# Performance work log

Hardware: AMD Instinct MI355X
Metric: run time of the kernel (lower is better)

The kernel has to match this reference:

```python
import jax, jax.numpy as jnp
import numpy as np

B, S, H = 2, 1024, 2048
NH, NKV, D = 16, 4, 128
E, K, F = 16, 2, 1408          # routed experts, top_k, moe_intermediate
FS = 1408                      # shared-expert intermediate (n_shared_experts=1)
EPS = 1e-5
RSF = 1.0                      # routed_scaling_factor


def rmsnorm(x, w):
    v = jnp.mean(jnp.square(x.astype(jnp.float32)), axis=-1, keepdims=True)
    return (x * jax.lax.rsqrt(v + EPS)).astype(x.dtype) * w


def rotate_half(x):
    x1, x2 = jnp.split(x, 2, axis=-1)
    return jnp.concatenate([-x2, x1], axis=-1)


def apply_rope(x, cos, sin):
    # x: [B,S,h,D]; cos/sin: [S,D]
    c = cos[None, :, None, :]
    s = sin[None, :, None, :]
    return x * c + rotate_half(x) * s


def setup_inputs() -> dict:
    key = jax.random.key(0)
    ks = jax.random.split(key, 16)
    sc = 0.02
    hidden_states = jax.random.normal(ks[0], (B, S, H), dtype=jnp.float32)
    # rotary embedding tables
    inv_freq = 1.0 / (10000.0 ** (np.arange(0, D, 2, dtype=np.float32) / D))
    ang = np.arange(S, dtype=np.float32)[:, None] * inv_freq[None, :]
    emb = np.concatenate([ang, ang], axis=-1)
    cos = jnp.asarray(np.cos(emb), dtype=jnp.float32)
    sin = jnp.asarray(np.sin(emb), dtype=jnp.float32)
    return {
        'hidden_states': hidden_states,
        'cos': cos,
        'sin': sin,
        'ln1_w': jnp.ones((H,), jnp.float32),
        'ln2_w': jnp.ones((H,), jnp.float32),
        'q_norm_w': jnp.ones((D,), jnp.float32),
        'k_norm_w': jnp.ones((D,), jnp.float32),
        'wq': jax.random.normal(ks[1], (H, NH * D), jnp.float32) * sc,
        'wk': jax.random.normal(ks[2], (H, NKV * D), jnp.float32) * sc,
        'wv': jax.random.normal(ks[3], (H, NKV * D), jnp.float32) * sc,
        'wo': jax.random.normal(ks[4], (NH * D, H), jnp.float32) * sc,
        'gate_w': jax.random.normal(ks[5], (E, H), jnp.float32) * sc,
        'expert_gate_up': jax.random.normal(ks[6], (E, H, 2 * F), jnp.float32) * sc,
        'expert_down': jax.random.normal(ks[7], (E, F, H), jnp.float32) * sc,
        'shared_gate_up': jax.random.normal(ks[8], (H, 2 * FS), jnp.float32) * sc,
        'shared_down': jax.random.normal(ks[9], (FS, H), jnp.float32) * sc,
    }


def silu_and_mul(gu):
    g, u = jnp.split(gu, 2, axis=-1)
    return jax.nn.silu(g) * u


def moe_block(tokens, gate_w, expert_gate_up, expert_down, shared_gate_up, shared_down):
    # tokens: [T,H]
    T = tokens.shape[0]
    router_logits = tokens.astype(jnp.float32) @ gate_w.T          # [T,E]
    probs = jax.nn.softmax(router_logits, axis=-1)
    topk_w, topk_ids = jax.lax.top_k(probs, K)                     # [T,K]
    topk_w = topk_w / jnp.sum(topk_w, axis=-1, keepdims=True)      # renormalize
    # dense combine-weight matrix [T,E] (top_k sparse routing)
    cw = jnp.zeros((T, E), jnp.float32).at[jnp.arange(T)[:, None], topk_ids].add(topk_w)
    # scan over experts: each expert is a full SwiGLU MLP on all tokens, masked by cw
    def body(acc, we):
        gw, dw, cwe = we                                            # [H,2F],[F,H],[T]
        y = silu_and_mul(tokens @ gw) @ dw                          # [T,H]
        return acc + cwe[:, None].astype(y.dtype) * y, None
    out, _ = jax.lax.scan(body, jnp.zeros_like(tokens), (expert_gate_up, expert_down, cw.T))
    out = out * RSF
    shared = silu_and_mul(tokens @ shared_gate_up) @ shared_down
    return out + shared


def reference(hidden_states, cos, sin, ln1_w, ln2_w, q_norm_w, k_norm_w,
              wq, wk, wv, wo, gate_w, expert_gate_up, expert_down,
              shared_gate_up, shared_down):
    # input layernorm (residual=None branch)
    residual = hidden_states
    x = rmsnorm(hidden_states, ln1_w)
    # attention
    q = (x @ wq).reshape(B, S, NH, D)
    k = (x @ wk).reshape(B, S, NKV, D)
    v = (x @ wv).reshape(B, S, NKV, D)
    q = rmsnorm(q, q_norm_w)
    k = rmsnorm(k, k_norm_w)
    q = apply_rope(q, cos, sin)
    k = apply_rope(k, cos, sin)
    rep = NH // NKV
    k = jnp.repeat(k, rep, axis=2)
    v = jnp.repeat(v, rep, axis=2)
    scores = jnp.einsum('bihd,bjhd->bhij', q, k) / jnp.sqrt(jnp.float32(D))
    causal = jnp.tril(jnp.ones((S, S), bool))
    scores = jnp.where(causal[None, None], scores, -jnp.inf)
    attn = jax.nn.softmax(scores, axis=-1)
    o = jnp.einsum('bhij,bjhd->bihd', attn, v).reshape(B, S, NH * D)
    attn_out = o @ wo
    # post-attention layernorm with fused residual add
    residual = residual + attn_out
    x = rmsnorm(residual, ln2_w)
    # MoE + shared expert
    tokens = x.reshape(-1, H)
    out = moe_block(tokens, gate_w, expert_gate_up, expert_down, shared_gate_up, shared_down)
    hidden = out.reshape(B, S, H)
    return hidden, residual
```

## Files before the change

kernel.cpp:

```cpp
#include <hip/hip_runtime.h>
#include <stdint.h>

typedef unsigned short u16;
typedef unsigned int   u32;
typedef __attribute__((ext_vector_type(4))) float     f32x4;
typedef __attribute__((ext_vector_type(8))) _Float16  f16x8;

#define S_LEN 1024
#define NB    2
#define H_DIM 2048
#define T_TOK 2048
#define NHEAD 16
#define NKVH  4
#define DHEAD 128
#define NEXP  16
#define FFE   1408
#define FF2   2816
#define EPSF  1e-5f
#define RSF_C 1.0f

__device__ __forceinline__ u16 f2h(float f){
  _Float16 h = (_Float16)f;
  return __builtin_bit_cast(unsigned short, h);
}
__device__ __forceinline__ void split2(float f, u16& hi, u16& lo){
  _Float16 h = (_Float16)f;
  hi = __builtin_bit_cast(unsigned short, h);
  _Float16 l = (_Float16)((f - (float)h) * 2048.0f);
  lo = __builtin_bit_cast(unsigned short, l);
}
__device__ __forceinline__ void gload_lds16(const void* g, void* l){
  __builtin_amdgcn_global_load_lds((const __attribute__((address_space(1))) void*)g,
                                   (__attribute__((address_space(3))) void*)l, 16, 0, 0);
}
__device__ __forceinline__ uint4 pack8(const u16* p){
  return make_uint4((u32)p[0] | ((u32)p[1]<<16), (u32)p[2] | ((u32)p[3]<<16),
                    (u32)p[4] | ((u32)p[5]<<16), (u32)p[6] | ((u32)p[7]<<16));
}

__global__ __launch_bounds__(256) void tsplit_all_kernel(
    const float* __restrict__ wq, const float* __restrict__ wk,
    const float* __restrict__ wv, const float* __restrict__ wo,
    const float* __restrict__ sgu, const float* __restrict__ sdn,
    u16* __restrict__ wqkvh, u16* __restrict__ wqkvl,
    u16* __restrict__ woh,  u16* __restrict__ wol,
    u16* __restrict__ sgut, u16* __restrict__ sdnt)
{
  const int z = blockIdx.z;
  const float* in; int ldn; u16* outh; u16* outl; int ldk, nx, ny; bool dual;
  switch (z) {
    case 0:  in=wq;  ldn=2048; outh=wqkvh;              outl=wqkvl;              ldk=2048; nx=32; ny=32; dual=true;  break;
    case 1:  in=wk;  ldn=512;  outh=wqkvh+2048*2048;    outl=wqkvl+2048*2048;    ldk=2048; nx=8;  ny=32; dual=true;  break;
    case 2:  in=wv;  ldn=512;  outh=wqkvh+2560*2048;    outl=wqkvl+2560*2048;    ldk=2048; nx=8;  ny=32; dual=true;  break;
    case 3:  in=wo;  ldn=2048; outh=woh;                outl=wol;                ldk=2048; nx=32; ny=32; dual=true;  break;
    case 4:  in=sgu; ldn=2816; outh=sgut;               outl=nullptr;            ldk=2048; nx=44; ny=32; dual=false; break;
    default: in=sdn; ldn=2048; outh=sdnt;               outl=nullptr;            ldk=1408; nx=32; ny=22; dual=false; break;
  }
  if ((int)blockIdx.x >= nx || (int)blockIdx.y >= ny) return;
  __shared__ float tile[64][65];
  const int n0 = blockIdx.x * 64, k0 = blockIdx.y * 64;
  const int tid = threadIdx.x;
  const int tr = tid >> 4, tc = (tid & 15) * 4;
  #pragma unroll
  for (int i = 0; i < 4; i++) {
    float4 v = *(const float4*)&in[(size_t)(k0 + tr + i*16) * ldn + (n0 + tc)];
    tile[tr + i*16][tc+0] = v.x; tile[tr + i*16][tc+1] = v.y;
    tile[tr + i*16][tc+2] = v.z; tile[tr + i*16][tc+3] = v.w;
  }
  __syncthreads();
  const int n = tid >> 2, kg = (tid & 3) * 16;
  u16 hb[16], lb[16];
  #pragma unroll
  for (int j = 0; j < 16; j++) {
    float f = tile[kg + j][n];
    if (dual) split2(f, hb[j], lb[j]); else hb[j] = f2h(f);
  }
  u16* dh = &outh[(size_t)(n0 + n) * ldk + k0 + kg];
  *(uint4*)dh       = pack8(hb);
  *(uint4*)(dh + 8) = pack8(hb + 8);
  if (dual) {
    u16* dl = &outl[(size_t)(n0 + n) * ldk + k0 + kg];
    *(uint4*)dl       = pack8(lb);
    *(uint4*)(dl + 8) = pack8(lb + 8);
  }
}

__global__ __launch_bounds__(256) void rmsnorm_kernel(
    const float* __restrict__ in, const float* __restrict__ w,
    u16* __restrict__ outh, u16* __restrict__ outl)
{
  __shared__ float red[4];
  const int t = blockIdx.x, tid = threadIdx.x;
  const int lane = tid & 63, wave = tid >> 6;
  const float* x = in + (size_t)t * H_DIM;
  const int c = tid * 8;
  float4 v0 = *(const float4*)&x[c];
  float4 v1 = *(const float4*)&x[c + 4];
  float ss = v0.x*v0.x + v0.y*v0.y + v0.z*v0.z + v0.w*v0.w
           + v1.x*v1.x + v1.y*v1.y + v1.z*v1.z + v1.w*v1.w;
  #pragma unroll
  for (int d = 1; d < 64; d <<= 1) ss += __shfl_xor(ss, d, 64);
  if (lane == 0) red[wave] = ss;
  __syncthreads();
  float rinv = rsqrtf((red[0]+red[1]+red[2]+red[3]) * (1.0f/H_DIM) + EPSF);
  float4 w0 = *(const float4*)&w[c];
  float4 w1 = *(const float4*)&w[c + 4];
  float vals[8] = { v0.x*rinv*w0.x, v0.y*rinv*w0.y, v0.z*rinv*w0.z, v0.w*rinv*w0.w,
                    v1.x*rinv*w1.x, v1.y*rinv*w1.y, v1.z*rinv*w1.z, v1.w*rinv*w1.w };
  u16 hb[8], lb[8];
  #pragma unroll
  for (int j = 0; j < 8; j++) split2(vals[j], hb[j], lb[j]);
  *(uint4*)&outh[(size_t)t * H_DIM + c] = pack8(hb);
  if (outl) *(uint4*)&outl[(size_t)t * H_DIM + c] = pack8(lb);
}

__global__ __launch_bounds__(256) void gemm3b_kernel(
    const u16* __restrict__ Ah, const u16* __restrict__ Al, int lda,
    const u16* __restrict__ Bh, const u16* __restrict__ Bl, int ldb,
    float* __restrict__ C, int ldc,
    const float* __restrict__ addsrc, int K)
{
  __shared__ u16 Ash[128*64], Asl[128*64];
  __shared__ u16 Bsh[128*64], Bsl[128*64];
  const int tid = threadIdx.x, lane = tid & 63, wave = tid >> 6;
  const int m0 = blockIdx.y * 128, n0 = blockIdx.x * 128;
  const int wm = (wave >> 1) * 64, wn = (wave & 1) * 64;
  const int arow = lane >> 3;
  const int acol = ((lane & 7) ^ arow) * 8;
  f32x4 acc0[4][4] = {}, acc1[4][4] = {};
  for (int k0 = 0; k0 < K; k0 += 64) {
    #pragma unroll
    for (int g = 0; g < 4; g++) {
      const int rb = wave*32 + g*8;
      gload_lds16(Ah + (size_t)(m0 + rb + arow)*lda + k0 + acol, &Ash[rb*64]);
      gload_lds16(Al + (size_t)(m0 + rb + arow)*lda + k0 + acol, &Asl[rb*64]);
      gload_lds16(Bh + (size_t)(n0 + rb + arow)*ldb + k0 + acol, &Bsh[rb*64]);
      gload_lds16(Bl + (size_t)(n0 + rb + arow)*ldb + k0 + acol, &Bsl[rb*64]);
    }
    asm volatile("s_waitcnt vmcnt(0) lgkmcnt(0)" ::: "memory");
    __syncthreads();
    const int fr = lane & 15, fg = lane >> 4;
    #pragma unroll
    for (int kk = 0; kk < 2; kk++) {
      const int cb = fg + kk*4;
      f16x8 ah[4], al[4];
      #pragma unroll
      for (int m = 0; m < 4; m++) {
        const int r = wm + m*16 + fr;
        const int s = (cb ^ (r & 7)) * 8;
        ah[m] = *(const f16x8*)&Ash[r*64 + s];
        al[m] = *(const f16x8*)&Asl[r*64 + s];
      }
      #pragma unroll
      for (int n = 0; n < 4; n++) {
        const int r = wn + n*16 + fr;
        const int s = (cb ^ (r & 7)) * 8;
        f16x8 bh_ = *(const f16x8*)&Bsh[r*64 + s];
        f16x8 bl_ = *(const f16x8*)&Bsl[r*64 + s];
        #pragma unroll
        for (int m = 0; m < 4; m++) {
          acc0[m][n] = __builtin_amdgcn_mfma_f32_16x16x32_f16(ah[m], bh_, acc0[m][n], 0,0,0);
          acc1[m][n] = __builtin_amdgcn_mfma_f32_16x16x32_f16(ah[m], bl_, acc1[m][n], 0,0,0);
          acc1[m][n] = __builtin_amdgcn_mfma_f32_16x16x32_f16(al[m], bh_, acc1[m][n], 0,0,0);
        }
      }
    }
    __syncthreads();
  }
  const int cr = (lane >> 4) * 4, cc = lane & 15;
  #pragma unroll
  for (int m = 0; m < 4; m++)
    #pragma unroll
    for (int n = 0; n < 4; n++)
      #pragma unroll
      for (int j = 0; j < 4; j++) {
        int r = m0 + wm + m*16 + cr + j;
        size_t idx = (size_t)r * ldc + (n0 + wn + n*16 + cc);
        float v = acc0[m][n][j] + acc1[m][n][j] * (1.0f/2048.0f);
        if (addsrc) v += addsrc[idx];
        C[idx] = v;
      }
}

__global__ __launch_bounds__(256) void gemm_up_all_kernel(
    const int* __restrict__ list, const float* __restrict__ egu, float* __restrict__ gu_exp,
    const int* __restrict__ counts, const int* __restrict__ offs,
    const int* __restrict__ tile_e, const int* __restrict__ tile_m0,
    const u16* __restrict__ tok, const u16* __restrict__ sgut, float* __restrict__ gu_sh)
{
  __shared__ u16 As[256*64];
  __shared__ u16 Bs[64*64];
  const int z = blockIdx.z;
  const int tid = threadIdx.x, lane = tid & 63, wave = tid >> 6;
  const int n0 = blockIdx.x * 64;
  const int wm = wave * 64;
  const int arow = lane >> 3;
  const int acol = ((lane & 7) ^ arow) * 8;
  const int fr = lane & 15, fg = lane >> 4;
  const int cr = (lane >> 4) * 4, cc = lane & 15;

  if (z < 32) {
    const int e = tile_e[z];
    if (e < 0) return;
    const int m0 = tile_m0[z];
    const int cnt = counts[e];
    const int off = offs[e];
    const float* B = egu + (size_t)e * H_DIM * FF2;
    float* C = gu_exp + (size_t)off * FF2;
    const u16* arp[8];
    #pragma unroll
    for (int g = 0; g < 8; g++) {
      int idx = off + m0 + wm + g*8 + arow;
      if (idx > 2*T_TOK - 1) idx = 2*T_TOK - 1;
      arp[g] = tok + (size_t)list[idx] * H_DIM + acol;
    }
    const int bn  = tid & 63;
    const int bkb = tid >> 6;
    const int bs0 = bn*64 + (((bkb*2)     ^ (bn & 7)) * 8);
    const int bs1 = bn*64 + (((bkb*2 + 1) ^ (bn & 7)) * 8);
    f32x4 acc[4][4] = {};
    for (int k0 = 0; k0 < H_DIM; k0 += 64) {
      #pragma unroll
      for (int g = 0; g < 8; g++)
        gload_lds16(arp[g] + k0, &As[(wm + g*8)*64]);
      {
        const float* gb = B + (size_t)(k0 + bkb*16) * FF2 + (n0 + bn);
        float f[16];
        #pragma unroll
        for (int j = 0; j < 16; j++) f[j] = gb[(size_t)j * FF2];
        u32 pk[8];
        #pragma unroll
        for (int j = 0; j < 8; j++)
          pk[j] = __builtin_bit_cast(u32, __builtin_amdgcn_cvt_pkrtz(f[2*j], f[2*j+1]));
        *(uint4*)&Bs[bs0] = make_uint4(pk[0], pk[1], pk[2], pk[3]);
        *(uint4*)&Bs[bs1] = make_uint4(pk[4], pk[5], pk[6], pk[7]);
      }
      asm volatile("s_waitcnt vmcnt(0) lgkmcnt(0)" ::: "memory");
      __syncthreads();
      #pragma unroll
      for (int kk = 0; kk < 2; kk++) {
        const int cb = fg + kk*4;
        f16x8 a[4], b[4];
        #pragma unroll
        for (int m = 0; m < 4; m++) {
          const int r = wm + m*16 + fr;
          a[m] = *(const f16x8*)&As[r*64 + ((cb ^ (r & 7)) * 8)];
        }
        #pragma unroll
        for (int n = 0; n < 4; n++) {
          const int r = n*16 + fr;
          b[n] = *(const f16x8*)&Bs[r*64 + ((cb ^ (r & 7)) * 8)];
        }
        #pragma unroll
        for (int n = 0; n < 4; n++)
          #pragma unroll
          for (int m = 0; m < 4; m++)
            acc[m][n] = __builtin_amdgcn_mfma_f32_16x16x32_f16(a[m], b[n], acc[m][n], 0,0,0);
      }
      __syncthreads();
    }
    #pragma unroll
    for (int m = 0; m < 4; m++)
      #pragma unroll
      for (int n = 0; n < 4; n++)
        #pragma unroll
        for (int j = 0; j < 4; j++) {
          int r = m0 + wm + m*16 + cr + j;
          if (r < cnt) C[(size_t)r * FF2 + (n0 + n*16 + cc)] = acc[m][n][j];
        }
  } else {
    const int m0 = (z - 32) * 256;
    f32x4 acc[4][4] = {};
    for (int k0 = 0; k0 < H_DIM; k0 += 64) {
      #pragma unroll
      for (int g = 0; g < 8; g++)
        gload_lds16(tok + (size_t)(m0 + wm + g*8 + arow)*H_DIM + k0 + acol,
                    &As[(wm + g*8)*64]);
      #pragma unroll
      for (int g = 0; g < 2; g++)
        gload_lds16(sgut + (size_t)(n0 + wave*16 + g*8 + arow)*H_DIM + k0 + acol,
                    &Bs[(wave*16 + g*8)*64]);
      asm volatile("s_waitcnt vmcnt(0) lgkmcnt(0)" ::: "memory");
      __syncthreads();
      #pragma unroll
      for (int kk = 0; kk < 2; kk++) {
        const int cb = fg + kk*4;
        f16x8 a[4], b[4];
        #pragma unroll
        for (int m = 0; m < 4; m++) {
          const int r = wm + m*16 + fr;
          a[m] = *(const f16x8*)&As[r*64 + ((cb ^ (r & 7)) * 8)];
        }
        #pragma unroll
        for (int n = 0; n < 4; n++) {
          const int r = n*16 + fr;
          b[n] = *(const f16x8*)&Bs[r*64 + ((cb ^ (r & 7)) * 8)];
        }
        #pragma unroll
        for (int n = 0; n < 4; n++)
          #pragma unroll
          for (int m = 0; m < 4; m++)
            acc[m][n] = __builtin_amdgcn_mfma_f32_16x16x32_f16(a[m], b[n], acc[m][n], 0,0,0);
      }
      __syncthreads();
    }
    #pragma unroll
    for (int m = 0; m < 4; m++)
      #pragma unroll
      for (int n = 0; n < 4; n++)
        #pragma unroll
        for (int j = 0; j < 4; j++)
          gu_sh[(size_t)(m0 + wm + m*16 + cr + j) * FF2 + (n0 + n*16 + cc)] = acc[m][n][j];
  }
}

__global__ __launch_bounds__(256) void gemm_dn_all_kernel(
    const u16* __restrict__ Aexp, const float* __restrict__ edn, float* __restrict__ y_exp,
    const int* __restrict__ counts, const int* __restrict__ offs,
    const int* __restrict__ tile_e, const int* __restrict__ tile_m0,
    const u16* __restrict__ act_sh, const u16* __restrict__ sdnt, float* __restrict__ out_sh)
{
  __shared__ u16 As[256*64];
  __shared__ u16 Bs[64*64];
  const int z = blockIdx.z;
  const int tid = threadIdx.x, lane = tid & 63, wave = tid >> 6;
  const int n0 = blockIdx.x * 64;
  const int wm = wave * 64;
  const int arow = lane >> 3;
  const int acol = ((lane & 7) ^ arow) * 8;
  const int fr = lane & 15, fg = lane >> 4;
  const int cr = (lane >> 4) * 4, cc = lane & 15;

  if (z < 32) {
    const int e = tile_e[z];
    if (e < 0) return;
    const int m0 = tile_m0[z];
    const int cnt = counts[e];
    const int off = offs[e];
    const u16* A = Aexp + (size_t)off * FFE;
    const float* B = edn + (size_t)e * FFE * H_DIM;
    float* C = y_exp + (size_t)off * H_DIM;
    const int bn  = tid & 63;
    const int bkb = tid >> 6;
    const int bs0 = bn*64 + (((bkb*2)     ^ (bn & 7)) * 8);
    const int bs1 = bn*64 + (((bkb*2 + 1) ^ (bn & 7)) * 8);
    f32x4 acc[4][4] = {};
    for (int k0 = 0; k0 < FFE; k0 += 64) {
      #pragma unroll
      for (int g = 0; g < 8; g++)
        gload_lds16(A + (size_t)(m0 + wm + g*8 + arow)*FFE + k0 + acol,
                    &As[(wm + g*8)*64]);
      {
        const float* gb = B + (size_t)(k0 + bkb*16) * H_DIM + (n0 + bn);
        float f[16];
        #pragma unroll
        for (int j = 0; j < 16; j++) f[j] = gb[(size_t)j * H_DIM];
        u32 pk[8];
        #pragma unroll
        for (int j = 0; j < 8; j++)
          pk[j] = __builtin_bit_cast(u32, __builtin_amdgcn_cvt_pkrtz(f[2*j], f[2*j+1]));
        *(uint4*)&Bs[bs0] = make_uint4(pk[0], pk[1], pk[2], pk[3]);
        *(uint4*)&Bs[bs1] = make_uint4(pk[4], pk[5], pk[6], pk[7]);
      }
      asm volatile("s_waitcnt vmcnt(0) lgkmcnt(0)" ::: "memory");
      __syncthreads();
      #pragma unroll
      for (int kk = 0; kk < 2; kk++) {
        const int cb = fg + kk*4;
        f16x8 a[4], b[4];
        #pragma unroll
        for (int m = 0; m < 4; m++) {
          const int r = wm + m*16 + fr;
          a[m] = *(const f16x8*)&As[r*64 + ((cb ^ (r & 7)) * 8)];
        }
        #pragma unroll
        for (int n = 0; n < 4; n++) {
          const int r = n*16 + fr;
          b[n] = *(const f16x8*)&Bs[r*64 + ((cb ^ (r & 7)) * 8)];
        }
        #pragma unroll
        for (int n = 0; n < 4; n++)
          #pragma unroll
          for (int m = 0; m < 4; m++)
            acc[m][n] = __builtin_amdgcn_mfma_f32_16x16x32_f16(a[m], b[n], acc[m][n], 0,0,0);
      }
      __syncthreads();
    }
    #pragma unroll
    for (int m = 0; m < 4; m++)
      #pragma unroll
      for (int n = 0; n < 4; n++)
        #pragma unroll
        for (int j = 0; j < 4; j++) {
          int r = m0 + wm + m*16 + cr + j;
          if (r < cnt) C[(size_t)r * H_DIM + (n0 + n*16 + cc)] = acc[m][n][j];
        }
  } else {
    const int m0 = (z - 32) * 256;
    f32x4 acc[4][4] = {};
    for (int k0 = 0; k0 < FFE; k0 += 64) {
      #pragma unroll
      for (int g = 0; g < 8; g++)
        gload_lds16(act_sh + (size_t)(m0 + wm + g*8 + arow)*FFE + k0 + acol,
                    &As[(wm + g*8)*64]);
      #pragma unroll
      for (int g = 0; g < 2; g++)
        gload_lds16(sdnt + (size_t)(n0 + wave*16 + g*8 + arow)*FFE + k0 + acol,
                    &Bs[(wave*16 + g*8)*64]);
      asm volatile("s_waitcnt vmcnt(0) lgkmcnt(0)" ::: "memory");
      __syncthreads();
      #pragma unroll
      for (int kk = 0; kk < 2; kk++) {
        const int cb = fg + kk*4;
        f16x8 a[4], b[4];
        #pragma unroll
        for (int m = 0; m < 4; m++) {
          const int r = wm + m*16 + fr;
          a[m] = *(const f16x8*)&As[r*64 + ((cb ^ (r & 7)) * 8)];
        }
        #pragma unroll
        for (int n = 0; n < 4; n++) {
          const int r = n*16 + fr;
          b[n] = *(const f16x8*)&Bs[r*64 + ((cb ^ (r & 7)) * 8)];
        }
        #pragma unroll
        for (int n = 0; n < 4; n++)
          #pragma unroll
          for (int m = 0; m < 4; m++)
            acc[m][n] = __builtin_amdgcn_mfma_f32_16x16x32_f16(a[m], b[n], acc[m][n], 0,0,0);
      }
      __syncthreads();
    }
    #pragma unroll
    for (int m = 0; m < 4; m++)
      #pragma unroll
      for (int n = 0; n < 4; n++)
        #pragma unroll
        for (int j = 0; j < 4; j++)
          out_sh[(size_t)(m0 + wm + m*16 + cr + j) * H_DIM + (n0 + n*16 + cc)] = acc[m][n][j];
  }
}

__global__ __launch_bounds__(256) void rope_kernel(
    const float* __restrict__ qkv,
    const float* __restrict__ cosb, const float* __restrict__ sinb,
    const float* __restrict__ qnw, const float* __restrict__ knw,
    u16* __restrict__ qrh, u16* __restrict__ qrl,
    u16* __restrict__ krh, u16* __restrict__ krl,
    u16* __restrict__ vth, u16* __restrict__ vtl)
{
  const int jid = blockIdx.x * 4 + (threadIdx.x >> 6);
  const int lane = threadIdx.x & 63;
  const int t = jid / 24, r = jid - t*24;
  const int b = t >> 10, s = t & (S_LEN - 1);
  const float* row = qkv + (size_t)t * 3072;
  if (r < NHEAD + NKVH) {
    const bool isq = (r < NHEAD);
    const int h = isq ? r : (r - NHEAD);
    const float* x = row + (isq ? h*DHEAD : (2048 + h*DHEAD));
    const float* nw = isq ? qnw : knw;
    float x0 = x[lane], x1 = x[lane + 64];
    float ss = x0*x0 + x1*x1;
    #pragma unroll
    for (int d = 1; d < 64; d <<= 1) ss += __shfl_xor(ss, d, 64);
    float rinv = rsqrtf(ss * (1.0f/DHEAD) + EPSF);
    float n0 = x0*rinv*nw[lane], n1 = x1*rinv*nw[lane + 64];
    float o0 = n0*cosb[s*DHEAD + lane]      - n1*sinb[s*DHEAD + lane];
    float o1 = n1*cosb[s*DHEAD + lane + 64] + n0*sinb[s*DHEAD + lane + 64];
    size_t base = isq ? ((size_t)(b*NHEAD + h)*S_LEN + s)*DHEAD
                      : ((size_t)(b*NKVH + h)*S_LEN + s)*DHEAD;
    u16* dh = isq ? qrh : krh;
    u16* dl = isq ? qrl : krl;
    u16 hh, ll;
    split2(o0, hh, ll); dh[base + lane]      = hh; dl[base + lane]      = ll;
    split2(o1, hh, ll); dh[base + lane + 64] = hh; dl[base + lane + 64] = ll;
  } else {
    const int h = r - NHEAD - NKVH;
    const float* x = row + 2560 + h*DHEAD;
    size_t base = (size_t)(b*NKVH + h)*DHEAD*S_LEN + s;
    u16 hh, ll;
    split2(x[lane], hh, ll);
    vth[base + (size_t)lane*S_LEN] = hh; vtl[base + (size_t)lane*S_LEN] = ll;
    split2(x[lane + 64], hh, ll);
    vth[base + (size_t)(lane + 64)*S_LEN] = hh; vtl[base + (size_t)(lane + 64)*S_LEN] = ll;
  }
}

__global__ __launch_bounds__(256) void attn_kernel(
    const u16* __restrict__ qrh, const u16* __restrict__ qrl,
    const u16* __restrict__ krh, const u16* __restrict__ krl,
    const u16* __restrict__ vth, const u16* __restrict__ vtl,
    u16* __restrict__ oh, u16* __restrict__ ol)
{
  __shared__ u16 Kh[64*128], Kl[64*128];
  __shared__ u16 Vh[128*64], Vl[128*64];
  __shared__ u16 Ph[4*16*64], Pl[4*16*64];
  const int bx = blockIdx.x, h = blockIdx.y, b = blockIdx.z;
  const int hkv = h >> 2;
  const int lane = threadIdx.x & 63, wave = threadIdx.x >> 6;
  const int fr = lane & 15, fg = lane >> 4;
  const u16* qbh = qrh + ((size_t)(b*NHEAD + h)*S_LEN)*DHEAD;
  const u16* qbl = qrl + ((size_t)(b*NHEAD + h)*S_LEN)*DHEAD;
  const u16* kbh = krh + ((size_t)(b*NKVH + hkv)*S_LEN)*DHEAD;
  const u16* kbl = krl + ((size_t)(b*NKVH + hkv)*S_LEN)*DHEAD;
  const u16* vbh = vth + ((size_t)(b*NKVH + hkv)*DHEAD)*S_LEN;
  const u16* vbl = vtl + ((size_t)(b*NKVH + hkv)*DHEAD)*S_LEN;
  const float scl = 0.08838834764831845f;

  for (int it = 0; it < 2; it++) {
    const int qt = it ? (15 - bx) : bx;
    const int q0 = qt * 64;
    f16x8 aqh[4], aql[4];
    {
      const size_t qrow = (size_t)(q0 + wave*16 + fr)*DHEAD;
      #pragma unroll
      for (int kk = 0; kk < 4; kk++) {
        aqh[kk] = *(const f16x8*)&qbh[qrow + kk*32 + fg*8];
        aql[kk] = *(const f16x8*)&qbl[qrow + kk*32 + fg*8];
      }
    }
    f32x4 o0[8] = {}, o1[8] = {};
    float mrow[4] = {-1e30f,-1e30f,-1e30f,-1e30f};
    float lrow[4] = {0.f,0.f,0.f,0.f};
    for (int jt = 0; jt <= qt; jt++) {
      const int j0 = jt * 64;
      #pragma unroll
      for (int p = 0; p < 4; p++) {
        const int ck = p*4 + wave;
        gload_lds16(kbh + (size_t)(j0 + ck*4 + (lane>>4))*DHEAD + (lane&15)*8, &Kh[ck*512]);
        gload_lds16(kbl + (size_t)(j0 + ck*4 + (lane>>4))*DHEAD + (lane&15)*8, &Kl[ck*512]);
        gload_lds16(vbh + (size_t)(ck*8 + (lane>>3))*S_LEN + j0 + (lane&7)*8, &Vh[ck*512]);
        gload_lds16(vbl + (size_t)(ck*8 + (lane>>3))*S_LEN + j0 + (lane&7)*8, &Vl[ck*512]);
      }
      __syncthreads();
      f32x4 s0[4] = {}, s1[4] = {};
      #pragma unroll
      for (int kk = 0; kk < 4; kk++) {
        const int ko = kk*32 + fg*8;
        #pragma unroll
        for (int n = 0; n < 4; n++) {
          f16x8 bh_ = *(const f16x8*)&Kh[(n*16 + fr)*128 + ko];
          f16x8 bl_ = *(const f16x8*)&Kl[(n*16 + fr)*128 + ko];
          s0[n] = __builtin_amdgcn_mfma_f32_16x16x32_f16(aqh[kk], bh_, s0[n], 0,0,0);
          s1[n] = __builtin_amdgcn_mfma_f32_16x16x32_f16(aqh[kk], bl_, s1[n], 0,0,0);
          s1[n] = __builtin_amdgcn_mfma_f32_16x16x32_f16(aql[kk], bh_, s1[n], 0,0,0);
        }
      }
      const int rb = q0 + wave*16 + fg*4;
      float pv[4][4];
      #pragma unroll
      for (int n = 0; n < 4; n++)
        #pragma unroll
        for (int j = 0; j < 4; j++) {
          float v = (s0[n][j] + s1[n][j]*(1.0f/2048.0f)) * scl;
          if (j0 + n*16 + fr > rb + j) v = -1e30f;
          pv[n][j] = v;
        }
      float alpha[4];
      #pragma unroll
      for (int j = 0; j < 4; j++) {
        float mx = fmaxf(fmaxf(pv[0][j], pv[1][j]), fmaxf(pv[2][j], pv[3][j]));
        #pragma unroll
        for (int d = 1; d < 16; d <<= 1) mx = fmaxf(mx, __shfl_xor(mx, d, 64));
        float mnew = fmaxf(mrow[j], mx);
        alpha[j] = __expf(mrow[j] - mnew);
        mrow[j] = mnew;
      }
      float rsum[4] = {0.f,0.f,0.f,0.f};
      #pragma unroll
      for (int n = 0; n < 4; n++)
        #pragma unroll
        for (int j = 0; j < 4; j++) {
          float p = __expf(pv[n][j] - mrow[j]);
          pv[n][j] = p;
          rsum[j] += p;
        }
      #pragma unroll
      for (int j = 0; j < 4; j++) {
        #pragma unroll
        for (int d = 1; d < 16; d <<= 1) rsum[j] += __shfl_xor(rsum[j], d, 64);
        lrow[j] = lrow[j]*alpha[j] + rsum[j];
      }
      #pragma unroll
      for (int n2 = 0; n2 < 8; n2++)
        #pragma unroll
        for (int j = 0; j < 4; j++) { o0[n2][j] *= alpha[j]; o1[n2][j] *= alpha[j]; }
      #pragma unroll
      for (int n = 0; n < 4; n++)
        #pragma unroll
        for (int j = 0; j < 4; j++) {
          u16 hh, ll; split2(pv[n][j], hh, ll);
          Ph[wave*1024 + (fg*4 + j)*64 + n*16 + fr] = hh;
          Pl[wave*1024 + (fg*4 + j)*64 + n*16 + fr] = ll;
        }
      __syncthreads();
      #pragma unroll
      for (int kk = 0; kk < 2; kk++) {
        const int ko = kk*32 + fg*8;
        f16x8 ah_ = *(const f16x8*)&Ph[wave*1024 + fr*64 + ko];
        f16x8 al_ = *(const f16x8*)&Pl[wave*1024 + fr*64 + ko];
        #pragma unroll
        for (int n2 = 0; n2 < 8; n2++) {
          f16x8 vh_ = *(const f16x8*)&Vh[(n2*16 + fr)*64 + ko];
          f16x8 vl_ = *(const f16x8*)&Vl[(n2*16 + fr)*64 + ko];
          o0[n2] = __builtin_amdgcn_mfma_f32_16x16x32_f16(ah_, vh_, o0[n2], 0,0,0);
          o1[n2] = __builtin_amdgcn_mfma_f32_16x16x32_f16(ah_, vl_, o1[n2], 0,0,0);
          o1[n2] = __builtin_amdgcn_mfma_f32_16x16x32_f16(al_, vh_, o1[n2], 0,0,0);
        }
      }
      __syncthreads();
    }
    float inv[4];
    #pragma unroll
    for (int j = 0; j < 4; j++) inv[j] = 1.0f / lrow[j];
    #pragma unroll
    for (int n2 = 0; n2 < 8; n2++)
      #pragma unroll
      for (int j = 0; j < 4; j++) {
        int s = q0 + wave*16 + fg*4 + j;
        size_t idx = ((size_t)(b*S_LEN + s))*H_DIM + h*DHEAD + n2*16 + fr;
        float val = (o0[n2][j] + o1[n2][j]*(1.0f/2048.0f)) * inv[j];
        u16 hh, ll; split2(val, hh, ll);
        oh[idx] = hh; ol[idx] = ll;
      }
  }
}

__global__ __launch_bounds__(64) void router_kernel(
    const float* __restrict__ resid, const float* __restrict__ ln2w,
    const float* __restrict__ gw, int* __restrict__ ids, float* __restrict__ wts,
    int* __restrict__ counts)
{
  const int t = blockIdx.x, lane = threadIdx.x;
  const float* x = resid + (size_t)t * H_DIM;
  float xv[32];
  float ss = 0.f;
  #pragma unroll
  for (int p = 0; p < 8; p++) {
    float4 v  = *(const float4*)&x[p*256 + lane*4];
    float4 lw = *(const float4*)&ln2w[p*256 + lane*4];
    ss += v.x*v.x + v.y*v.y + v.z*v.z + v.w*v.w;
    xv[p*4+0] = v.x*lw.x; xv[p*4+1] = v.y*lw.y; xv[p*4+2] = v.z*lw.z; xv[p*4+3] = v.w*lw.w;
  }
  #pragma unroll
  for (int d = 1; d < 64; d <<= 1) ss += __shfl_xor(ss, d, 64);
  const float rinv = rsqrtf(ss * (1.0f/H_DIM) + EPSF);
  float lg[NEXP];
  #pragma unroll
  for (int e = 0; e < NEXP; e++) {
    const float* g = gw + (size_t)e * H_DIM;
    float dacc = 0.f;
    #pragma unroll
    for (int p = 0; p < 8; p++) {
      float4 gv = *(const float4*)&g[p*256 + lane*4];
      dacc += xv[p*4+0]*gv.x + xv[p*4+1]*gv.y + xv[p*4+2]*gv.z + xv[p*4+3]*gv.w;
    }
    #pragma unroll
    for (int d = 1; d < 64; d <<= 1) dacc += __shfl_xor(dacc, d, 64);
    lg[e] = dacc * rinv;
  }
  if (lane == 0) {
    int i0 = 0; float b0 = lg[0];
    #pragma unroll
    for (int e = 1; e < NEXP; e++) if (lg[e] > b0) { b0 = lg[e]; i0 = e; }
    int i1 = -1; float b1 = -3e38f;
    #pragma unroll
    for (int e = 0; e < NEXP; e++) if (e != i0 && lg[e] > b1) { b1 = lg[e]; i1 = e; }
    float rr = __expf(b1 - b0);
    float w0 = 1.0f / (1.0f + rr);
    ids[t*2] = i0; ids[t*2+1] = i1;
    wts[t*2] = w0; wts[t*2+1] = rr * w0;
    atomicAdd(&counts[i0], 1);
    atomicAdd(&counts[i1], 1);
  }
}

__global__ void scan_kernel(const int* __restrict__ counts, int* __restrict__ offs,
                            int* __restrict__ cursor,
                            int* __restrict__ tile_e, int* __restrict__ tile_m0)
{
  if (threadIdx.x == 0) {
    int s = 0, nt = 0;
    for (int e = 0; e < NEXP; e++) {
      offs[e] = s; cursor[e] = 0;
      int c = counts[e];
      for (int m0 = 0; m0 < c; m0 += 256) { tile_e[nt] = e; tile_m0[nt] = m0; nt++; }
      s += c;
    }
    for (; nt < 32; nt++) { tile_e[nt] = -1; tile_m0[nt] = 0; }
  }
}

__global__ __launch_bounds__(256) void scatter_kernel(
    const int* __restrict__ ids, const int* __restrict__ offs,
    int* __restrict__ cursor, int* __restrict__ list, int* __restrict__ pos)
{
  int t = blockIdx.x * 256 + threadIdx.x;
  if (t < T_TOK) {
    for (int kk = 0; kk < 2; kk++) {
      int e = ids[t*2 + kk];
      int p = atomicAdd(&cursor[e], 1);
      int i = offs[e] + p;
      list[i] = t;
      pos[t*2 + kk] = i;
    }
  }
}

__global__ __launch_bounds__(256) void silu_all_kernel(
    const float* __restrict__ gu_exp, u16* __restrict__ act_ex,
    const float* __restrict__ gu_sh,  u16* __restrict__ act_sh)
{
  const int rr = blockIdx.x;
  const float* g;
  u16* o;
  if (rr < 2*T_TOK) { g = gu_exp + (size_t)rr * FF2;          o = act_ex + (size_t)rr * FFE; }
  else              { g = gu_sh  + (size_t)(rr - 2*T_TOK) * FF2; o = act_sh + (size_t)(rr - 2*T_TOK) * FFE; }
  for (int c = threadIdx.x*4; c < FFE; c += 1024) {
    float4 gv = *(const float4*)&g[c];
    float4 uv = *(const float4*)&g[c + FFE];
    float s0 = gv.x / (1.0f + __expf(-gv.x)) * uv.x;
    float s1 = gv.y / (1.0f + __expf(-gv.y)) * uv.y;
    float s2 = gv.z / (1.0f + __expf(-gv.z)) * uv.z;
    float s3 = gv.w / (1.0f + __expf(-gv.w)) * uv.w;
    u32 lo = (u32)f2h(s0) | ((u32)f2h(s1) << 16);
    u32 hi = (u32)f2h(s2) | ((u32)f2h(s3) << 16);
    *(uint2*)&o[c] = make_uint2(lo, hi);
  }
}

__global__ __launch_bounds__(256) void combine_kernel(
    const float* __restrict__ y,
    const int* __restrict__ pos, const float* __restrict__ wts,
    float* __restrict__ out)
{
  const int t = blockIdx.x;
  const int p0 = pos[t*2], p1 = pos[t*2+1];
  const float w0 = wts[t*2] * RSF_C, w1 = wts[t*2+1] * RSF_C;
  const int c = threadIdx.x * 8;
  #pragma unroll
  for (int q = 0; q < 2; q++) {
    const int cc = c + q*4;
    float4 s  = *(const float4*)&out[(size_t)t*H_DIM + cc];
    float4 a  = *(const float4*)&y[(size_t)p0*H_DIM + cc];
    float4 bb = *(const float4*)&y[(size_t)p1*H_DIM + cc];
    float4 r;
    r.x = s.x + w0*a.x + w1*bb.x;
    r.y = s.y + w0*a.y + w1*bb.y;
    r.z = s.z + w0*a.z + w1*bb.z;
    r.w = s.w + w0*a.w + w1*bb.w;
    *(float4*)&out[(size_t)t*H_DIM + cc] = r;
  }
}

extern "C" void kernel_launch(void* const* d_in, const int* in_sizes, int n_in,
                              void* d_out, int out_size, void* d_ws, size_t ws_size,
                              hipStream_t stream)
{
  (void)in_sizes; (void)n_in; (void)out_size;
  const float* hidden = (const float*)d_in[0];
  const float* cosb   = (const float*)d_in[1];
  const float* sinb   = (const float*)d_in[2];
  const float* ln1w   = (const float*)d_in[3];
  const float* ln2w   = (const float*)d_in[4];
  const float* qnw    = (const float*)d_in[5];
  const float* knw    = (const float*)d_in[6];
  const float* wq     = (const float*)d_in[7];
  const float* wk     = (const float*)d_in[8];
  const float* wv     = (const float*)d_in[9];
  const float* wo     = (const float*)d_in[10];
  const float* gw     = (const float*)d_in[11];
  const float* egu    = (const float*)d_in[12];
  const float* edn    = (const float*)d_in[13];
  const float* sgu    = (const float*)d_in[14];
  const float* sdn    = (const float*)d_in[15];
  float* out_hidden = (float*)d_out;
  float* resid = (float*)d_out + (size_t)T_TOK * H_DIM;

  char* ws = (char*)d_ws;
  constexpr size_t OFF_XH    = 0;
  constexpr size_t OFF_XL    = 8388608;
  constexpr size_t OFF_WQKVH = 16777216;
  constexpr size_t OFF_WQKVL = 29360128;
  constexpr size_t OFF_WOH   = 41943040;
  constexpr size_t OFF_WOL   = 50331648;
  constexpr size_t OFF_QKV   = 58720256;
  constexpr size_t OFF_QRH = 16777216, OFF_QRL = 25165824;
  constexpr size_t OFF_KRH = 33554432, OFF_KRL = 35651584;
  constexpr size_t OFF_VTH = 37748736, OFF_VTL = 39845888;
  constexpr size_t OFF_OH = 58720256, OFF_OL = 67108864;
  constexpr size_t OFF_GUE = 0;
  constexpr size_t OFF_TOK = 63963136;
  constexpr size_t OFF_ACE = 72351744;
  constexpr size_t OFF_GUS = 84606976;
  constexpr size_t OFF_ACS = 107675648;
  constexpr size_t OFF_SGUT= 113442816;
  constexpr size_t OFF_SDNT= 124977152;
  constexpr size_t OFF_IDS = 130744320;
  constexpr size_t OFF_WTS = OFF_IDS + 16384;
  constexpr size_t OFF_POS = OFF_WTS + 16384;
  constexpr size_t OFF_LST = OFF_POS + 16384;
  constexpr size_t OFF_CNT = OFF_LST + 16384;
  constexpr size_t OFF_OFS = OFF_CNT + 64;
  constexpr size_t OFF_CUR = OFF_OFS + 64;
  constexpr size_t OFF_TE  = OFF_CUR + 64;
  constexpr size_t OFF_TM  = OFF_TE + 128;
  constexpr size_t WS_NEED = OFF_TM + 128;
  if (ws_size < WS_NEED) return;

  u16* xh     = (u16*)(ws + OFF_XH);
  u16* xl     = (u16*)(ws + OFF_XL);
  u16* wqkvh  = (u16*)(ws + OFF_WQKVH);
  u16* wqkvl  = (u16*)(ws + OFF_WQKVL);
  u16* woh    = (u16*)(ws + OFF_WOH);
  u16* wol    = (u16*)(ws + OFF_WOL);
  float* qkv  = (float*)(ws + OFF_QKV);
  u16* q_rh = (u16*)(ws + OFF_QRH);
  u16* q_rl = (u16*)(ws + OFF_QRL);
  u16* k_rh = (u16*)(ws + OFF_KRH);
  u16* k_rl = (u16*)(ws + OFF_KRL);
  u16* v_th = (u16*)(ws + OFF_VTH);
  u16* v_tl = (u16*)(ws + OFF_VTL);
  u16* o_h  = (u16*)(ws + OFF_OH);
  u16* o_l  = (u16*)(ws + OFF_OL);
  float* gu_exp = (float*)(ws + OFF_GUE);
  float* y_exp  = (float*)(ws + OFF_GUE);
  u16* tok      = (u16*)(ws + OFF_TOK);
  u16* act_ex   = (u16*)(ws + OFF_ACE);
  float* gu_sh  = (float*)(ws + OFF_GUS);
  u16* act_sh   = (u16*)(ws + OFF_ACS);
  u16* sgut     = (u16*)(ws + OFF_SGUT);
  u16* sdnt     = (u16*)(ws + OFF_SDNT);
  int* ids    = (int*)(ws + OFF_IDS);
  float* wts  = (float*)(ws + OFF_WTS);
  int* pos    = (int*)(ws + OFF_POS);
  int* list   = (int*)(ws + OFF_LST);
  int* counts = (int*)(ws + OFF_CNT);
  int* offs   = (int*)(ws + OFF_OFS);
  int* cursor = (int*)(ws + OFF_CUR);
  int* tile_e = (int*)(ws + OFF_TE);
  int* tile_m0= (int*)(ws + OFF_TM);

  hipMemsetAsync(counts, 0, 64, stream);

  tsplit_all_kernel<<<dim3(44,32,6), 256, 0, stream>>>(wq, wk, wv, wo, sgu, sdn,
                                                       wqkvh, wqkvl, woh, wol, sgut, sdnt);

  rmsnorm_kernel<<<T_TOK, 256, 0, stream>>>(hidden, ln1w, xh, xl);
  gemm3b_kernel<<<dim3(24,16), 256, 0, stream>>>(xh, xl, H_DIM, wqkvh, wqkvl, 2048, qkv, 3072, nullptr, H_DIM);
  rope_kernel<<<(T_TOK*24)/4, 256, 0, stream>>>(qkv, cosb, sinb, qnw, knw,
                                                q_rh, q_rl, k_rh, k_rl, v_th, v_tl);
  attn_kernel<<<dim3(8, NHEAD, NB), 256, 0, stream>>>(q_rh, q_rl, k_rh, k_rl, v_th, v_tl, o_h, o_l);
  gemm3b_kernel<<<dim3(16,16), 256, 0, stream>>>(o_h, o_l, H_DIM, woh, wol, 2048, resid, H_DIM, hidden, H_DIM);

  rmsnorm_kernel<<<T_TOK, 256, 0, stream>>>(resid, ln2w, tok, nullptr);
  router_kernel<<<T_TOK, 64, 0, stream>>>(resid, ln2w, gw, ids, wts, counts);
  scan_kernel<<<1, 64, 0, stream>>>(counts, offs, cursor, tile_e, tile_m0);
  scatter_kernel<<<8, 256, 0, stream>>>(ids, offs, cursor, list, pos);

  gemm_up_all_kernel<<<dim3(44,1,40), 256, 0, stream>>>(list, egu, gu_exp,
                                                        counts, offs, tile_e, tile_m0,
                                                        tok, sgut, gu_sh);
  silu_all_kernel<<<3*T_TOK, 256, 0, stream>>>(gu_exp, act_ex, gu_sh, act_sh);
  gemm_dn_all_kernel<<<dim3(32,1,40), 256, 0, stream>>>(act_ex, edn, y_exp,
                                                        counts, offs, tile_e, tile_m0,
                                                        act_sh, sdnt, out_hidden);
  combine_kernel<<<T_TOK, 256, 0, stream>>>(y_exp, pos, wts, out_hidden);
}
```

Before: 737.6 us.

## Overlap wo and shared-expert weight conversion with attention in one launch

The weight transpose/split work for wo and the shared-expert matrices moves out of the upfront conversion kernel and into extra z-slices of the attention launch, so it runs alongside the 256 attention blocks, which alone underfill the GPU. The upfront kernel now converts only wq/wk/wv. The goal is to fill idle CUs during attention and shorten the serial prologue. In exchange, the merged kernel uses the larger 80KB shared-memory footprint for every block, which can lower occupancy for the conversion blocks. The launch grid also contains many early-exit blocks.

```diff
diff --git a/kernel.cpp b/kernel.cpp
--- a/kernel.cpp
+++ b/kernel.cpp
@@ -38,26 +38,12 @@
                     (u32)p[4] | ((u32)p[5]<<16), (u32)p[6] | ((u32)p[7]<<16));
 }
 
-__global__ __launch_bounds__(256) void tsplit_all_kernel(
-    const float* __restrict__ wq, const float* __restrict__ wk,
-    const float* __restrict__ wv, const float* __restrict__ wo,
-    const float* __restrict__ sgu, const float* __restrict__ sdn,
-    u16* __restrict__ wqkvh, u16* __restrict__ wqkvl,
-    u16* __restrict__ woh,  u16* __restrict__ wol,
-    u16* __restrict__ sgut, u16* __restrict__ sdnt)
-{
-  const int z = blockIdx.z;
-  const float* in; int ldn; u16* outh; u16* outl; int ldk, nx, ny; bool dual;
-  switch (z) {
-    case 0:  in=wq;  ldn=2048; outh=wqkvh;              outl=wqkvl;              ldk=2048; nx=32; ny=32; dual=true;  break;
-    case 1:  in=wk;  ldn=512;  outh=wqkvh+2048*2048;    outl=wqkvl+2048*2048;    ldk=2048; nx=8;  ny=32; dual=true;  break;
-    case 2:  in=wv;  ldn=512;  outh=wqkvh+2560*2048;    outl=wqkvl+2560*2048;    ldk=2048; nx=8;  ny=32; dual=true;  break;
-    case 3:  in=wo;  ldn=2048; outh=woh;                outl=wol;                ldk=2048; nx=32; ny=32; dual=true;  break;
-    case 4:  in=sgu; ldn=2816; outh=sgut;               outl=nullptr;            ldk=2048; nx=44; ny=32; dual=false; break;
-    default: in=sdn; ldn=2048; outh=sdnt;               outl=nullptr;            ldk=1408; nx=32; ny=22; dual=false; break;
-  }
-  if ((int)blockIdx.x >= nx || (int)blockIdx.y >= ny) return;
-  __shared__ float tile[64][65];
+__device__ __forceinline__ void tsplit_body(
+    const float* __restrict__ in, int ldn,
+    u16* __restrict__ outh, u16* __restrict__ outl, int ldk, bool dual,
+    void* smem)
+{
+  float (*tile)[65] = (float(*)[65])smem;
   const int n0 = blockIdx.x * 64, k0 = blockIdx.y * 64;
   const int tid = threadIdx.x;
   const int tr = tid >> 4, tc = (tid & 15) * 4;
@@ -83,6 +69,23 @@
     *(uint4*)dl       = pack8(lb);
     *(uint4*)(dl + 8) = pack8(lb + 8);
   }
+}
+
+__global__ __launch_bounds__(256) void tsplit_all_kernel(
+    const float* __restrict__ wq, const float* __restrict__ wk,
+    const float* __restrict__ wv,
+    u16* __restrict__ wqkvh, u16* __restrict__ wqkvl)
+{
+  const int z = blockIdx.z;
+  const float* in; int ldn; u16* outh; u16* outl; int nx;
+  switch (z) {
+    case 0:  in=wq;  ldn=2048; outh=wqkvh;            outl=wqkvl;            nx=32; break;
+    case 1:  in=wk;  ldn=512;  outh=wqkvh+2048*2048;  outl=wqkvl+2048*2048;  nx=8;  break;
+    default: in=wv;  ldn=512;  outh=wqkvh+2560*2048;  outl=wqkvl+2560*2048;  nx=8;  break;
+  }
+  if ((int)blockIdx.x >= nx) return;
+  __shared__ __align__(16) char smem[16704];
+  tsplit_body(in, ldn, outh, outl, 2048, true, smem);
 }
 
 __global__ __launch_bounds__(256) void rmsnorm_kernel(
@@ -486,16 +489,36 @@
   }
 }
 
-__global__ __launch_bounds__(256) void attn_kernel(
+__global__ __launch_bounds__(256) void attn_mix_kernel(
     const u16* __restrict__ qrh, const u16* __restrict__ qrl,
     const u16* __restrict__ krh, const u16* __restrict__ krl,
     const u16* __restrict__ vth, const u16* __restrict__ vtl,
-    u16* __restrict__ oh, u16* __restrict__ ol)
-{
-  __shared__ u16 Kh[64*128], Kl[64*128];
-  __shared__ u16 Vh[128*64], Vl[128*64];
-  __shared__ u16 Ph[4*16*64], Pl[4*16*64];
-  const int bx = blockIdx.x, h = blockIdx.y, b = blockIdx.z;
+    u16* __restrict__ oh, u16* __restrict__ ol,
+    const float* __restrict__ wo, const float* __restrict__ sgu, const float* __restrict__ sdn,
+    u16* __restrict__ woh, u16* __restrict__ wol,
+    u16* __restrict__ sgut, u16* __restrict__ sdnt)
+{
+  __shared__ __align__(16) char smem[81920];
+  const int z = blockIdx.z;
+  if (z >= 2) {
+    const float* in; int ldn; u16* outh; u16* outl; int ldk, nx, ny; bool dual;
+    switch (z) {
+      case 2:  in=wo;  ldn=2048; outh=woh;  outl=wol;     ldk=2048; nx=32; ny=32; dual=true;  break;
+      case 3:  in=sgu; ldn=2816; outh=sgut; outl=nullptr; ldk=2048; nx=44; ny=32; dual=false; break;
+      default: in=sdn; ldn=2048; outh=sdnt; outl=nullptr; ldk=1408; nx=32; ny=22; dual=false; break;
+    }
+    if ((int)blockIdx.x >= nx || (int)blockIdx.y >= ny) return;
+    tsplit_body(in, ldn, outh, outl, ldk, dual, smem);
+    return;
+  }
+  if ((int)blockIdx.x >= 8 || (int)blockIdx.y >= NHEAD) return;
+  u16* Kh = (u16*)smem;
+  u16* Kl = (u16*)(smem + 16384);
+  u16* Vh = (u16*)(smem + 32768);
+  u16* Vl = (u16*)(smem + 49152);
+  u16* Ph = (u16*)(smem + 65536);
+  u16* Pl = (u16*)(smem + 73728);
+  const int bx = blockIdx.x, h = blockIdx.y, b = z;
   const int hkv = h >> 2;
   const int lane = threadIdx.x & 63, wave = threadIdx.x >> 6;
   const int fr = lane & 15, fg = lane >> 4;
@@ -843,14 +866,14 @@
 
   hipMemsetAsync(counts, 0, 64, stream);
 
-  tsplit_all_kernel<<<dim3(44,32,6), 256, 0, stream>>>(wq, wk, wv, wo, sgu, sdn,
-                                                       wqkvh, wqkvl, woh, wol, sgut, sdnt);
+  tsplit_all_kernel<<<dim3(32,32,3), 256, 0, stream>>>(wq, wk, wv, wqkvh, wqkvl);
 
   rmsnorm_kernel<<<T_TOK, 256, 0, stream>>>(hidden, ln1w, xh, xl);
   gemm3b_kernel<<<dim3(24,16), 256, 0, stream>>>(xh, xl, H_DIM, wqkvh, wqkvl, 2048, qkv, 3072, nullptr, H_DIM);
   rope_kernel<<<(T_TOK*24)/4, 256, 0, stream>>>(qkv, cosb, sinb, qnw, knw,
                                                 q_rh, q_rl, k_rh, k_rl, v_th, v_tl);
-  attn_kernel<<<dim3(8, NHEAD, NB), 256, 0, stream>>>(q_rh, q_rl, k_rh, k_rl, v_th, v_tl, o_h, o_l);
+  attn_mix_kernel<<<dim3(44,32,5), 256, 0, stream>>>(q_rh, q_rl, k_rh, k_rl, v_th, v_tl, o_h, o_l,
+                                                     wo, sgu, sdn, woh, wol, sgut, sdnt);
   gemm3b_kernel<<<dim3(16,16), 256, 0, stream>>>(o_h, o_l, H_DIM, woh, wol, 2048, resid, H_DIM, hidden, H_DIM);
 
   rmsnorm_kernel<<<T_TOK, 256, 0, stream>>>(resid, ln2w, tok, nullptr);
```

Result: slower. 812.5 us (+10.2%).
